# Performance work log

Hardware: AMD Instinct MI355X
Metric: run time of the kernel (lower is better)

Reference implementation:

```python
import jax, jax.numpy as jnp
import numpy as np

G, K = 4, 3
P = K * K  # n_offset_points


def _conv(x, w, b, groups=1):
    # x: [B,C,H,W] NCHW, w: [O, I/groups, kh, kw] (torch OIHW), padding=1 -> SAME
    y = jax.lax.conv_general_dilated(x, w, (1, 1), 'SAME', feature_group_count=groups)
    return y + b[None, :, None, None]


def setup_inputs() -> dict:
    key = jax.random.key(0)
    ks = jax.random.split(key, 9)
    B, C, H, W = 4, 256, 64, 64
    Cg = C // G
    s = 0.05
    return {
        'x': jax.random.normal(ks[0], (B, H * W, C), jnp.float32),
        'off_w1': jax.random.normal(ks[1], (C, Cg, 3, 3), jnp.float32) * s,
        'off_b1': jax.random.normal(ks[2], (C,), jnp.float32) * s,
        'off_w2': jax.random.normal(ks[3], (G * 2 * P, C, 3, 3), jnp.float32) * s,
        'off_b2': jax.random.normal(ks[4], (G * 2 * P,), jnp.float32) * s,
        'mod_w1': jax.random.normal(ks[5], (C // 4, C, 3, 3), jnp.float32) * s,
        'mod_b1': jax.random.normal(ks[6], (C // 4,), jnp.float32) * s,
        'mod_w2': jax.random.normal(ks[7], (G * P, C // 4, 3, 3), jnp.float32) * s,
        'mod_b2': jax.random.normal(ks[8], (G * P,), jnp.float32) * s,
        'H': 64,
        'W': 64,
    }


def reference(x, off_w1, off_b1, off_w2, off_b2, mod_w1, mod_b1, mod_w2, mod_b2, H, W):
    B, N, C = x.shape
    Cg = C // G
    x2d = x.transpose(0, 2, 1).reshape(B, C, H, W)

    # offset branch (grouped 3x3 conv -> GELU -> 3x3 conv), offset_scale = 1.0
    h = jax.nn.gelu(_conv(x2d, off_w1, off_b1, groups=G), approximate=False)
    off = _conv(h, off_w2, off_b2).reshape(B, G, 2, P, H, W)
    # modulation branch
    m = jax.nn.gelu(_conv(x2d, mod_w1, mod_b1), approximate=False)
    mod = jax.nn.sigmoid(_conv(m, mod_w2, mod_b2)).reshape(B, G, P, H, W)

    # base kernel offsets: base[0]=x, base[1]=y, each [P]
    rv = jnp.arange(-(K - 1) // 2, (K - 1) // 2 + 1, dtype=x.dtype)
    by, bx = jnp.meshgrid(rv, rv, indexing='ij')
    bx, by = bx.reshape(P), by.reshape(P)

    yg, xg = jnp.meshgrid(jnp.arange(H, dtype=x.dtype), jnp.arange(W, dtype=x.dtype), indexing='ij')
    # sampling coords in pixel space; clamp to [-1,1] normalized (align_corners=True)
    # is exactly clamp to [0, W-1] / [0, H-1] in pixel space, and border padding
    # then never goes out of range.
    px = jnp.clip(xg + bx[:, None, None] + off[:, :, 0], 0.0, W - 1)  # [B,G,P,H,W]
    py = jnp.clip(yg + by[:, None, None] + off[:, :, 1], 0.0, H - 1)

    x0f, y0f = jnp.floor(px), jnp.floor(py)
    wx, wy = px - x0f, py - y0f
    x0 = x0f.astype(jnp.int32)
    y0 = y0f.astype(jnp.int32)
    x1 = jnp.minimum(x0 + 1, W - 1)
    y1 = jnp.minimum(y0 + 1, H - 1)

    flat = x2d.reshape(B, G, Cg, H * W)

    def gather(yi, xi):
        idx = (yi * W + xi).reshape(B, G, 1, P, H * W)
        return jnp.take_along_axis(flat[:, :, :, None, :], idx, axis=-1)  # [B,G,Cg,P,HW]

    wxr = wx.reshape(B, G, 1, P, H * W)
    wyr = wy.reshape(B, G, 1, P, H * W)
    v = (gather(y0, x0) * (1 - wxr) * (1 - wyr)
         + gather(y0, x1) * wxr * (1 - wyr)
         + gather(y1, x0) * (1 - wxr) * wyr
         + gather(y1, x1) * wxr * wyr)
    v = v * mod.reshape(B, G, 1, P, H * W)
    out = v.mean(axis=3)  # average over offset points -> [B,G,Cg,HW]
    return out.reshape(B, C, H * W).transpose(0, 2, 1)
```

## Files before the change

kernel.cpp:

```cpp
#include <hip/hip_runtime.h>
#include <math.h>


#define SLAB 4369
#define AGAP 1056
#define APXS 40
#define AROW (66*APXS)
#define AHALF (6*AROW)

typedef __attribute__((ext_vector_type(8))) short short8;
typedef __attribute__((ext_vector_type(4))) float floatx4;

__device__ __forceinline__ unsigned short f2bf(float f) {
    unsigned u = __float_as_uint(f);
    u = (u + 0x7FFFu + ((u >> 16) & 1u)) >> 16;
    return (unsigned short)u;
}
__device__ __forceinline__ float bf2f(unsigned short h) {
    return __uint_as_float(((unsigned)h) << 16);
}
__device__ __forceinline__ void split2(float v, unsigned short* hi, unsigned short* lo) {
    unsigned short h = f2bf(v);
    *hi = h;
    *lo = f2bf(v - bf2f(h));
}
__device__ __forceinline__ float gelu_exact(float v) {
    return 0.5f * v * (1.0f + erff(v * 0.70710678118654752f));
}

template<int NC, int NTAPS, int NT, int ACT, int OUTMODE>
__device__ __forceinline__ void conv_core_lds(
    unsigned short* lds,
    const unsigned short* __restrict__ ah, const unsigned short* __restrict__ al,
    int aC0,
    const unsigned short* __restrict__ wh, const unsigned short* __restrict__ wl,
    const float* __restrict__ bias,
    int b, int mblock, int tap0,
    unsigned short* __restrict__ oh, unsigned short* __restrict__ ol,
    int oC0,
    float* __restrict__ pf)
{
    const int OCPAD = NT * 16;
    unsigned short* Ahl = lds;
    unsigned short* All = lds + AHALF;
    unsigned short* Bhl = lds + 2 * AHALF;
    unsigned short* Bll = lds + 2 * AHALF + OCPAD * APXS;

    int tid = (int)threadIdx.x;
    int wave = tid >> 6;
    int lane = tid & 63;
    int quad = lane >> 4;
    int l16 = lane & 15;

    int pix0 = (mblock * 4 + wave) * 64;
    int y0 = mblock * 4;

    floatx4 acc[4][NT];
#pragma unroll
    for (int nt = 0; nt < NT; nt++) {
        float bv = (OUTMODE == 1) ? bias[nt * 16 + l16] : 0.f;
#pragma unroll
        for (int mt = 0; mt < 4; mt++) { floatx4 v = {bv, bv, bv, bv}; acc[mt][nt] = v; }
    }

#pragma unroll 1
    for (int ch = 0; ch < NC; ch++) {
        {
            size_t gbase = ((size_t)((aC0 + ch) * 4 + b) * SLAB + (size_t)y0 * 66) * 32;
#pragma unroll
            for (int k = 0; k < 7; k++) {
                int u = k * 256 + tid;
                if (u < 1584) {
                    int px = u >> 2, j = u & 3;
                    int row = px / 66, col = px - row * 66;
                    int dst = row * AROW + col * APXS + j * 8;
                    *(short8*)(Ahl + dst) = *(const short8*)(ah + gbase + (size_t)u * 8);
                    *(short8*)(All + dst) = *(const short8*)(al + gbase + (size_t)u * 8);
                }
            }
        }
#pragma unroll 1
        for (int tp = 0; tp < NTAPS; tp++) {
            int tap = tap0 + tp;
            int kh = tap / 3, kw = tap - kh * 3;
            {
                size_t wbase = (size_t)(ch * 9 + tap) * OCPAD * 32;
                const int BU = OCPAD * 4;
#pragma unroll
                for (int k = 0; k * 256 < BU; k++) {
                    int u = k * 256 + tid;
                    if (u < BU) {
                        int oc = u >> 2, j = u & 3;
                        int dst = oc * APXS + j * 8;
                        *(short8*)(Bhl + dst) = *(const short8*)(wh + wbase + (size_t)u * 8);
                        *(short8*)(Bll + dst) = *(const short8*)(wl + wbase + (size_t)u * 8);
                    }
                }
            }
            __syncthreads();

            short8 Afh[4], Afl[4], Bfh[NT], Bfl[NT];
            int arow = (wave + kh) * AROW;
#pragma unroll
            for (int mt = 0; mt < 4; mt++) {
                int aoff = arow + (kw + l16 + mt * 16) * APXS + quad * 8;
                Afh[mt] = *(const short8*)(Ahl + aoff);
                Afl[mt] = *(const short8*)(All + aoff);
            }
#pragma unroll
            for (int nt = 0; nt < NT; nt++) {
                int boff = (nt * 16 + l16) * APXS + quad * 8;
                Bfh[nt] = *(const short8*)(Bhl + boff);
                Bfl[nt] = *(const short8*)(Bll + boff);
            }
#pragma unroll
            for (int nt = 0; nt < NT; nt++) {
#pragma unroll
                for (int mt = 0; mt < 4; mt++) {
                    acc[mt][nt] = __builtin_amdgcn_mfma_f32_16x16x32_bf16(Afh[mt], Bfh[nt], acc[mt][nt], 0, 0, 0);
                    acc[mt][nt] = __builtin_amdgcn_mfma_f32_16x16x32_bf16(Afh[mt], Bfl[nt], acc[mt][nt], 0, 0, 0);
                    acc[mt][nt] = __builtin_amdgcn_mfma_f32_16x16x32_bf16(Afl[mt], Bfh[nt], acc[mt][nt], 0, 0, 0);
                }
            }
            __syncthreads();
        }
    }

#pragma unroll
    for (int nt = 0; nt < NT; nt++) {
        int oc = nt * 16 + l16;
#pragma unroll
        for (int mt = 0; mt < 4; mt++) {
#pragma unroll
            for (int r = 0; r < 4; r++) {
                float v = acc[mt][nt][r];
                int px = pix0 + mt * 16 + quad * 4 + r;
                if (OUTMODE == 2) {
                    atomicAdd(pf + ((size_t)b * 4096 + px) * OCPAD + oc, v);
                } else if (OUTMODE == 3) {
                    pf[((size_t)b * 4096 + px) * OCPAD + oc] = v;
                } else {
                    if (ACT == 1) v = gelu_exact(v);
                    else if (ACT == 2) v = 1.0f / (1.0f + expf(-v));
                    int yy = (px >> 6) + 1, xx = (px & 63) + 1;
                    int och = oC0 + (oc >> 5);
                    size_t o = ((size_t)(och * 4 + b) * SLAB + yy * 66 + xx) * 32 + (oc & 31);
                    unsigned short hv, lv; split2(v, &hv, &lv);
                    oh[o] = hv; ol[o] = lv;
                }
            }
        }
    }
}

__global__ __launch_bounds__(256, 1) void convA_kernel(
    const unsigned short* __restrict__ xph, const unsigned short* __restrict__ xpl,
    const unsigned short* __restrict__ w1h, const unsigned short* __restrict__ w1l,
    const float* __restrict__ off_b1,
    const unsigned short* __restrict__ w3h, const unsigned short* __restrict__ w3l,
    unsigned short* __restrict__ h1h, unsigned short* __restrict__ h1l,
    float* __restrict__ P3)
{
    __shared__ unsigned short lds[2 * AHALF + 2 * 64 * APXS];
    int bx = blockIdx.x;
    int xcd = bx & 7;
    int j = bx >> 3;
    int pair = xcd * 8 + j / 7;
    int role = j % 7;
    int mb = pair & 15;
    int b = pair >> 4;
    if (role < 4) {
        int g = role;
        conv_core_lds<2, 9, 4, 1, 1>(lds, xph, xpl, g * 2,
            w1h + (size_t)g * 2 * 9 * 64 * 32, w1l + (size_t)g * 2 * 9 * 64 * 32,
            off_b1 + g * 64,
            b, mb, 0, h1h, h1l, g * 2, nullptr);
    } else {
        int ks = role - 4;
        conv_core_lds<8, 3, 4, 0, 2>(lds, xph, xpl, 0, w3h, w3l, nullptr,
            b, mb, ks * 3, nullptr, nullptr, 0, P3);
    }
}

__global__ __launch_bounds__(256) void finalizeA_kernel(
    const float* __restrict__ P3, const float* __restrict__ mod_b1,
    unsigned short* __restrict__ m1h, unsigned short* __restrict__ m1l)
{
    int idx = blockIdx.x * 256 + threadIdx.x;
    int c = idx & 63;
    int p = idx >> 6;
    int b = p >> 12;
    int px = p & 4095;
    int rem = ((px >> 6) + 1) * 66 + (px & 63) + 1;
    float u = P3[(size_t)p * 64 + c] + mod_b1[c];
    u = gelu_exact(u);
    size_t o = ((size_t)((c >> 5) * 4 + b) * SLAB + rem) * 32 + (c & 31);
    unsigned short hu, lu; split2(u, &hu, &lu);
    m1h[o] = hu; m1l[o] = lu;
}

__global__ __launch_bounds__(256, 1) void convB_kernel(
    const unsigned short* __restrict__ h1h, const unsigned short* __restrict__ h1l,
    const unsigned short* __restrict__ w2h, const unsigned short* __restrict__ w2l,
    const unsigned short* __restrict__ m1h, const unsigned short* __restrict__ m1l,
    const unsigned short* __restrict__ w4h, const unsigned short* __restrict__ w4l,
    float* __restrict__ P2a, float* __restrict__ P4a)
{
    __shared__ unsigned short lds[2 * AHALF + 2 * 80 * APXS];
    int bx = blockIdx.x;
    if (bx < 192) {
        int xcd = bx & 7;
        int j = bx >> 3;
        int pair = xcd * 8 + j / 3;
        int ks = j % 3;
        int mb = pair & 15;
        int b = pair >> 4;
        conv_core_lds<8, 3, 5, 0, 2>(lds, h1h, h1l, 0, w2h, w2l, nullptr,
            b, mb, ks * 3, nullptr, nullptr, 0, P2a);
    } else {
        int t = bx - 192;
        int xcd = t & 7;
        int q = t >> 3;
        int pair = xcd * 8 + q;
        int mb = pair & 15;
        int b = pair >> 4;
        conv_core_lds<2, 9, 3, 0, 3>(lds, m1h, m1l, 0, w4h, w4l, nullptr,
            b, mb, 0, nullptr, nullptr, 0, P4a);
    }
}

#define ZBLK 2304
#define RBLK 1040
#define XBLK 17424
#define WBLK 1980
__global__ void prep_all_kernel(
    const float* __restrict__ x,
    const float* __restrict__ w1f, const float* __restrict__ w2f,
    const float* __restrict__ w3f, const float* __restrict__ w4f,
    unsigned short* __restrict__ xph, unsigned short* __restrict__ xpl,
    unsigned short* __restrict__ h1h, unsigned short* __restrict__ h1l,
    unsigned short* __restrict__ m1h, unsigned short* __restrict__ m1l,
    unsigned short* __restrict__ w1h, unsigned short* __restrict__ w1l,
    unsigned short* __restrict__ w2h, unsigned short* __restrict__ w2l,
    unsigned short* __restrict__ w3h, unsigned short* __restrict__ w3l,
    unsigned short* __restrict__ w4h, unsigned short* __restrict__ w4l,
    float* __restrict__ accf)
{
    int blk = blockIdx.x;
    int t = threadIdx.x;
    if (blk < ZBLK) {
        ((uint4*)accf)[(size_t)blk * 256 + t] = make_uint4(0u, 0u, 0u, 0u);
        return;
    }
    blk -= ZBLK;
    if (blk < RBLK) {
        int b = blk / 260;
        int r = blk - b * 260;
        int i, j;
        if (r < 66)       { i = 0;        j = r; }
        else if (r < 132) { i = 65;       j = r - 66; }
        else if (r < 196) { i = r - 131;  j = 0; }
        else              { i = r - 195;  j = 65; }
        size_t pp = (size_t)i * 66 + j;
        int ch = t >> 5, sub = t & 31;
        size_t o = ((size_t)(ch * 4 + b) * SLAB + pp) * 32 + sub;
        h1h[o] = 0; h1l[o] = 0;
        if (t < 64) { m1h[o] = 0; m1l[o] = 0; }
        return;
    }
    blk -= RBLK;
    if (blk < XBLK) {
        int b = blk / 4356;
        int rem = blk - b * 4356;
        int i = rem / 66, j = rem - i * 66;
        float v = 0.f;
        if (i >= 1 && i <= 64 && j >= 1 && j <= 64)
            v = x[((size_t)b * 4096 + (size_t)(i - 1) * 64 + (j - 1)) * 256 + t];
        size_t o = ((size_t)((t >> 5) * 4 + b) * SLAB + rem) * 32 + (t & 31);
        unsigned short h, l; split2(v, &h, &l);
        xph[o] = h; xpl[o] = l;
        return;
    }
    blk -= XBLK;
    {
        const int N1 = 147456, N2 = 184320, N3 = 147456, N4 = 27648;
        int idx = blk * 256 + t;
        const float* w; unsigned short *outh, *outl;
        int ocpad, oc_real, ic, base;
        if (idx < N1)                { w = w1f; outh = w1h; outl = w1l; ocpad = 64; oc_real = 64; ic = 64;  base = 0; }
        else if (idx < N1 + N2)      { w = w2f; outh = w2h; outl = w2l; ocpad = 80; oc_real = 72; ic = 256; base = N1; }
        else if (idx < N1 + N2 + N3) { w = w3f; outh = w3h; outl = w3l; ocpad = 64; oc_real = 64; ic = 256; base = N1 + N2; }
        else                         { w = w4f; outh = w4h; outl = w4l; ocpad = 48; oc_real = 36; ic = 64;  base = N1 + N2 + N3; }
        int lidx = idx - base;
        int ici = lidx & 31;
        int t1 = lidx >> 5;
        int ocp = t1 % ocpad;
        int t2 = t1 / ocpad;
        int tap = t2 % 9;
        int t3 = t2 / 9;
        int nch = ic >> 5;
        int ch = t3 % nch;
        int g = t3 / nch;
        float v = 0.f;
        if (ocp < oc_real) {
            int oc = g * oc_real + ocp;
            int icx = ch * 32 + ici;
            v = w[((size_t)oc * ic + icx) * 9 + tap];
        }
        unsigned short h, l; split2(v, &h, &l);
        outh[lidx] = h; outl[lidx] = l;
    }
}

__global__ __launch_bounds__(256) void deform_sample(
    const float* __restrict__ x,
    const float* __restrict__ P2a, const float* __restrict__ P4a,
    const float* __restrict__ b2, const float* __restrict__ b4,
    float* __restrict__ out)
{
    int bid = (int)((blockIdx.x & 7u) * 512u + (blockIdx.x >> 3));
    int wid = (int)(((unsigned)bid * 256u + threadIdx.x) >> 6);
    int lane = (int)(threadIdx.x & 63u);
    int sub = lane >> 4;
    int li = lane & 15;

    int b = wid >> 12;
    int rem = wid & 4095;
    int g = rem >> 10;
    int hw = ((rem & 1023) << 2) + sub;
    int hy = hw >> 6;
    int wx = hw & 63;

    float fx = 0.f, fy = 0.f, fm = 0.f;
    if (li < 9) {
        size_t p = (size_t)(b << 12) + hw;
        int c2 = g * 18 + li;
        fx = P2a[p * 80 + c2] + b2[c2];
        fy = P2a[p * 80 + 9 + c2] + b2[9 + c2];
        int c4 = g * 9 + li;
        float mv = P4a[p * 48 + c4] + b4[c4];
        fm = 1.0f / (1.0f + expf(-mv));
    }
    float px = fminf(fmaxf((float)wx + (float)(li % 3 - 1) + fx, 0.f), 63.f);
    float py = fminf(fmaxf((float)hy + (float)(li / 3 - 1) + fy, 0.f), 63.f);
    float x0f = floorf(px), y0f = floorf(py);
    float wxf = px - x0f, wyf = py - y0f;
    int x0 = (int)x0f, y0 = (int)y0f;
    int x1 = min(x0 + 1, 63), y1 = min(y0 + 1, 63);

    const float4* xb = (const float4*)(x + ((size_t)(b << 12)) * 256 + g * 64 + li * 4);
    float4 acc = make_float4(0.f, 0.f, 0.f, 0.f);
    int sb = sub << 4;
#pragma unroll
    for (int q = 0; q < 9; q++) {
        int src = sb + q;
        int   qx0 = __shfl(x0, src);
        int   qx1 = __shfl(x1, src);
        int   qy0 = __shfl(y0, src);
        int   qy1 = __shfl(y1, src);
        float qwx = __shfl(wxf, src);
        float qwy = __shfl(wyf, src);
        float qm  = __shfl(fm, src);
        float4 v00 = xb[(size_t)(qy0 * 64 + qx0) * 64];
        float4 v01 = xb[(size_t)(qy0 * 64 + qx1) * 64];
        float4 v10 = xb[(size_t)(qy1 * 64 + qx0) * 64];
        float4 v11 = xb[(size_t)(qy1 * 64 + qx1) * 64];
        float w00 = (1.f - qwx) * (1.f - qwy);
        float w01 = qwx * (1.f - qwy);
        float w10 = (1.f - qwx) * qwy;
        float w11 = qwx * qwy;
        acc.x += qm * (v00.x * w00 + v01.x * w01 + v10.x * w10 + v11.x * w11);
        acc.y += qm * (v00.y * w00 + v01.y * w01 + v10.y * w10 + v11.y * w11);
        acc.z += qm * (v00.z * w00 + v01.z * w01 + v10.z * w10 + v11.z * w11);
        acc.w += qm * (v00.w * w00 + v01.w * w01 + v10.w * w10 + v11.w * w11);
    }
    const float s = 1.f / 9.f;
    acc.x *= s; acc.y *= s; acc.z *= s; acc.w *= s;
    float4* ob = (float4*)(out + ((size_t)(b << 12) + hw) * 256 + g * 64 + li * 4);
    *ob = acc;
}

extern "C" void kernel_launch(void* const* d_in, const int* in_sizes, int n_in,
                              void* d_out, int out_size, void* d_ws, size_t ws_size,
                              hipStream_t stream)
{
    const float* x      = (const float*)d_in[0];
    const float* off_w1 = (const float*)d_in[1];
    const float* off_b1 = (const float*)d_in[2];
    const float* off_w2 = (const float*)d_in[3];
    const float* off_b2 = (const float*)d_in[4];
    const float* mod_w1 = (const float*)d_in[5];
    const float* mod_b1 = (const float*)d_in[6];
    const float* mod_w2 = (const float*)d_in[7];
    const float* mod_b2 = (const float*)d_in[8];

    const size_t XP = 8u * 4u * SLAB * 32u;
    const size_t MP = 2u * 4u * SLAB * 32u;
    const size_t W1 = 4u * 2u * 9u * 64u * 32u;
    const size_t W2 = 8u * 9u * 80u * 32u;
    const size_t W3 = 8u * 9u * 64u * 32u;
    const size_t W4 = 2u * 9u * 48u * 32u;

    unsigned short* ws = (unsigned short*)d_ws;
    size_t o = 0;
    unsigned short* xph = ws + o; o += XP + AGAP;
    unsigned short* xpl = ws + o; o += XP + AGAP;
    unsigned short* h1h = ws + o; o += XP + AGAP;
    unsigned short* h1l = ws + o; o += XP + AGAP;
    unsigned short* m1h = ws + o; o += MP + AGAP;
    unsigned short* m1l = ws + o; o += MP + AGAP;
    unsigned short* w1h = ws + o; o += W1 + AGAP;
    unsigned short* w1l = ws + o; o += W1 + AGAP;
    unsigned short* w2h = ws + o; o += W2 + AGAP;
    unsigned short* w2l = ws + o; o += W2 + AGAP;
    unsigned short* w3h = ws + o; o += W3 + AGAP;
    unsigned short* w3l = ws + o; o += W3 + AGAP;
    unsigned short* w4h = ws + o; o += W4 + AGAP;
    unsigned short* w4l = ws + o; o += W4 + AGAP;
    o += o & 1;
    float* fbase = (float*)(ws + o);
    float* P3  = fbase;
    float* P2a = P3 + (size_t)4 * 4096 * 64;
    float* P4a = P2a + (size_t)4 * 4096 * 80;
    const size_t ACC_FLOATS = (size_t)4 * 4096 * (64 + 80 + 48);
    size_t need_bytes = o * 2 + ACC_FLOATS * 4;
    if (ws_size < need_bytes) return;

    prep_all_kernel<<<ZBLK + RBLK + XBLK + WBLK, 256, 0, stream>>>(
        x, off_w1, off_w2, mod_w1, mod_w2,
        xph, xpl, h1h, h1l, m1h, m1l,
        w1h, w1l, w2h, w2l, w3h, w3l, w4h, w4l, P3);

    convA_kernel<<<dim3(448, 1, 1), 256, 0, stream>>>(xph, xpl, w1h, w1l, off_b1,
                                                      w3h, w3l, h1h, h1l, P3);
    finalizeA_kernel<<<4096, 256, 0, stream>>>(P3, mod_b1, m1h, m1l);
    convB_kernel<<<dim3(256, 1, 1), 256, 0, stream>>>(h1h, h1l, w2h, w2l,
                                                      m1h, m1l, w4h, w4l, P2a, P4a);
    deform_sample<<<4096, 256, 0, stream>>>(x, P2a, P4a, off_b2, mod_b2, (float*)d_out);
}
```

Before: 216.6 us.

## Prefetch conv tiles through registers, double-buffer weights, split channels across more blocks

The conv core now issues global loads for the next channel's input tile and the next tap's weights into registers before running the current MFMAs. It then writes them to LDS afterwards, with weights double-buffered when BDBUF is set. Split-K blocks load only the 4 input rows they need. Both conv kernels split the channel dimension in half (and the mod_w2 conv by tap row), which raises grid sizes from 448/256 to 640/576 blocks. More blocks atomically add into the same outputs, so the zero-init block count grows. The cost is more register pressure and more atomic traffic.

New measurement: 224.7 us. 3.7% more time.

```diff
diff --git a/kernel.cpp b/kernel.cpp
--- a/kernel.cpp
+++ b/kernel.cpp
@@ -6,7 +6,6 @@
 #define AGAP 1056
 #define APXS 40
 #define AROW (66*APXS)
-#define AHALF (6*AROW)
 
 typedef __attribute__((ext_vector_type(8))) short short8;
 typedef __attribute__((ext_vector_type(4))) float floatx4;
@@ -28,12 +27,13 @@
     return 0.5f * v * (1.0f + erff(v * 0.70710678118654752f));
 }
 
-template<int NC, int NTAPS, int NT, int ACT, int OUTMODE>
+template<int NC, int NTAPS, int NT, int NROWS, int BDBUF, int ACT, int OUTMODE>
 __device__ __forceinline__ void conv_core_lds(
     unsigned short* lds,
     const unsigned short* __restrict__ ah, const unsigned short* __restrict__ al,
     int aC0,
     const unsigned short* __restrict__ wh, const unsigned short* __restrict__ wl,
+    int wC0,
     const float* __restrict__ bias,
     int b, int mblock, int tap0,
     unsigned short* __restrict__ oh, unsigned short* __restrict__ ol,
@@ -41,10 +41,17 @@
     float* __restrict__ pf)
 {
     const int OCPAD = NT * 16;
+    const int AHALFN = NROWS * AROW;
+    const int AU = NROWS * 66 * 4;
+    const int KA = (AU + 255) / 256;
+    const int BU = OCPAD * 4;
+    const int KB = (BU + 255) / 256;
+    const int BHALF = OCPAD * APXS;
+    const int BBUF = 2 * BHALF;
+
     unsigned short* Ahl = lds;
-    unsigned short* All = lds + AHALF;
-    unsigned short* Bhl = lds + 2 * AHALF;
-    unsigned short* Bll = lds + 2 * AHALF + OCPAD * APXS;
+    unsigned short* All = lds + AHALFN;
+    unsigned short* Bb  = lds + 2 * AHALFN;
 
     int tid = (int)threadIdx.x;
     int wave = tid >> 6;
@@ -52,8 +59,9 @@
     int quad = lane >> 4;
     int l16 = lane & 15;
 
+    int y0 = mblock * 4;
+    int row0 = (NROWS == 4) ? (tap0 / 3) : 0;
     int pix0 = (mblock * 4 + wave) * 64;
-    int y0 = mblock * 4;
 
     floatx4 acc[4][NT];
 #pragma unroll
@@ -63,44 +71,85 @@
         for (int mt = 0; mt < 4; mt++) { floatx4 v = {bv, bv, bv, bv}; acc[mt][nt] = v; }
     }
 
+    short8 ARh[KA], ARl[KA], BRh[KB], BRl[KB];
+
+    auto issueA = [&](int ch) {
+        size_t gbase = ((size_t)((aC0 + ch) * 4 + b) * SLAB + (size_t)(y0 + row0) * 66) * 32;
+#pragma unroll
+        for (int k = 0; k < KA; k++) {
+            int u = k * 256 + tid;
+            if (u < AU) {
+                ARh[k] = *(const short8*)(ah + gbase + (size_t)u * 8);
+                ARl[k] = *(const short8*)(al + gbase + (size_t)u * 8);
+            }
+        }
+    };
+    auto writeA = [&]() {
+#pragma unroll
+        for (int k = 0; k < KA; k++) {
+            int u = k * 256 + tid;
+            if (u < AU) {
+                int px = u >> 2, j = u & 3;
+                int row = px / 66, col = px - row * 66;
+                int dst = row * AROW + col * APXS + j * 8;
+                *(short8*)(Ahl + dst) = ARh[k];
+                *(short8*)(All + dst) = ARl[k];
+            }
+        }
+    };
+    auto issueB = [&](int it) {
+        int ch_ = it / NTAPS, tap_ = tap0 + it % NTAPS;
+        size_t wbase = ((size_t)((wC0 + ch_) * 9 + tap_)) * OCPAD * 32;
+#pragma unroll
+        for (int k = 0; k < KB; k++) {
+            int u = k * 256 + tid;
+            if (u < BU) {
+                BRh[k] = *(const short8*)(wh + wbase + (size_t)u * 8);
+                BRl[k] = *(const short8*)(wl + wbase + (size_t)u * 8);
+            }
+        }
+    };
+    auto writeB = [&](int sel) {
+        unsigned short* bh = Bb + sel * BBUF;
+        unsigned short* bl = bh + BHALF;
+#pragma unroll
+        for (int k = 0; k < KB; k++) {
+            int u = k * 256 + tid;
+            if (u < BU) {
+                int oc = u >> 2, j = u & 3;
+                int dst = oc * APXS + j * 8;
+                *(short8*)(bh + dst) = BRh[k];
+                *(short8*)(bl + dst) = BRl[k];
+            }
+        }
+    };
+
+    issueA(0);
+    issueB(0);
+    __builtin_amdgcn_sched_barrier(0);
+    writeA();
+    writeB(0);
+    __syncthreads();
+
+    int bsel = 0;
 #pragma unroll 1
     for (int ch = 0; ch < NC; ch++) {
-        {
-            size_t gbase = ((size_t)((aC0 + ch) * 4 + b) * SLAB + (size_t)y0 * 66) * 32;
-#pragma unroll
-            for (int k = 0; k < 7; k++) {
-                int u = k * 256 + tid;
-                if (u < 1584) {
-                    int px = u >> 2, j = u & 3;
-                    int row = px / 66, col = px - row * 66;
-                    int dst = row * AROW + col * APXS + j * 8;
-                    *(short8*)(Ahl + dst) = *(const short8*)(ah + gbase + (size_t)u * 8);
-                    *(short8*)(All + dst) = *(const short8*)(al + gbase + (size_t)u * 8);
-                }
-            }
-        }
-#pragma unroll 1
+#pragma unroll
         for (int tp = 0; tp < NTAPS; tp++) {
+            int it = ch * NTAPS + tp;
+            const bool chEnd = (tp == NTAPS - 1);
+            const bool lastIt = (ch == NC - 1) && chEnd;
+            if (!lastIt) {
+                if (chEnd) issueA(ch + 1);
+                issueB(it + 1);
+                __builtin_amdgcn_sched_barrier(0);
+            }
             int tap = tap0 + tp;
-            int kh = tap / 3, kw = tap - kh * 3;
-            {
-                size_t wbase = (size_t)(ch * 9 + tap) * OCPAD * 32;
-                const int BU = OCPAD * 4;
-#pragma unroll
-                for (int k = 0; k * 256 < BU; k++) {
-                    int u = k * 256 + tid;
-                    if (u < BU) {
-                        int oc = u >> 2, j = u & 3;
-                        int dst = oc * APXS + j * 8;
-                        *(short8*)(Bhl + dst) = *(const short8*)(wh + wbase + (size_t)u * 8);
-                        *(short8*)(Bll + dst) = *(const short8*)(wl + wbase + (size_t)u * 8);
-                    }
-                }
-            }
-            __syncthreads();
-
+            int kw = tap % 3;
+            int arow = ((NROWS == 6) ? (wave + tap / 3) : wave) * AROW;
+            unsigned short* bh = Bb + bsel * BBUF;
+            unsigned short* bl = bh + BHALF;
             short8 Afh[4], Afl[4], Bfh[NT], Bfl[NT];
-            int arow = (wave + kh) * AROW;
 #pragma unroll
             for (int mt = 0; mt < 4; mt++) {
                 int aoff = arow + (kw + l16 + mt * 16) * APXS + quad * 8;
@@ -110,8 +159,8 @@
 #pragma unroll
             for (int nt = 0; nt < NT; nt++) {
                 int boff = (nt * 16 + l16) * APXS + quad * 8;
-                Bfh[nt] = *(const short8*)(Bhl + boff);
-                Bfl[nt] = *(const short8*)(Bll + boff);
+                Bfh[nt] = *(const short8*)(bh + boff);
+                Bfl[nt] = *(const short8*)(bl + boff);
             }
 #pragma unroll
             for (int nt = 0; nt < NT; nt++) {
@@ -122,7 +171,20 @@
                     acc[mt][nt] = __builtin_amdgcn_mfma_f32_16x16x32_bf16(Afl[mt], Bfh[nt], acc[mt][nt], 0, 0, 0);
                 }
             }
-            __syncthreads();
+            if (!lastIt) {
+                if (BDBUF && !chEnd) {
+                    writeB(bsel ^ 1);
+                    __syncthreads();
+                    bsel ^= 1;
+                } else {
+                    __syncthreads();
+                    int ns = BDBUF ? (bsel ^ 1) : 0;
+                    writeB(ns);
+                    if (chEnd) writeA();
+                    __syncthreads();
+                    bsel = ns;
+                }
+            }
         }
     }
 
@@ -161,23 +223,25 @@
     unsigned short* __restrict__ h1h, unsigned short* __restrict__ h1l,
     float* __restrict__ P3)
 {
-    __shared__ unsigned short lds[2 * AHALF + 2 * 64 * APXS];
+    __shared__ unsigned short lds[36800];
     int bx = blockIdx.x;
     int xcd = bx & 7;
     int j = bx >> 3;
-    int pair = xcd * 8 + j / 7;
-    int role = j % 7;
+    int pair = xcd * 8 + j / 10;
+    int role = j % 10;
     int mb = pair & 15;
     int b = pair >> 4;
     if (role < 4) {
         int g = role;
-        conv_core_lds<2, 9, 4, 1, 1>(lds, xph, xpl, g * 2,
-            w1h + (size_t)g * 2 * 9 * 64 * 32, w1l + (size_t)g * 2 * 9 * 64 * 32,
+        conv_core_lds<2, 9, 4, 6, 0, 1, 1>(lds, xph, xpl, g * 2,
+            w1h + (size_t)g * 2 * 9 * 64 * 32, w1l + (size_t)g * 2 * 9 * 64 * 32, 0,
             off_b1 + g * 64,
             b, mb, 0, h1h, h1l, g * 2, nullptr);
     } else {
-        int ks = role - 4;
-        conv_core_lds<8, 3, 4, 0, 2>(lds, xph, xpl, 0, w3h, w3l, nullptr,
+        int r = role - 4;
+        int ks = r % 3, half = r / 3;
+        conv_core_lds<4, 3, 4, 4, 1, 0, 2>(lds, xph, xpl, half * 4,
+            w3h, w3l, half * 4, nullptr,
             b, mb, ks * 3, nullptr, nullptr, 0, P3);
     }
 }
@@ -206,30 +270,28 @@
     const unsigned short* __restrict__ w4h, const unsigned short* __restrict__ w4l,
     float* __restrict__ P2a, float* __restrict__ P4a)
 {
-    __shared__ unsigned short lds[2 * AHALF + 2 * 80 * APXS];
+    __shared__ unsigned short lds[33920];
     int bx = blockIdx.x;
-    if (bx < 192) {
-        int xcd = bx & 7;
-        int j = bx >> 3;
-        int pair = xcd * 8 + j / 3;
-        int ks = j % 3;
-        int mb = pair & 15;
-        int b = pair >> 4;
-        conv_core_lds<8, 3, 5, 0, 2>(lds, h1h, h1l, 0, w2h, w2l, nullptr,
+    int xcd = bx & 7;
+    int j = bx >> 3;
+    int pair = xcd * 8 + j / 9;
+    int role = j % 9;
+    int mb = pair & 15;
+    int b = pair >> 4;
+    if (role < 6) {
+        int ks = role % 3, half = role / 3;
+        conv_core_lds<4, 3, 5, 4, 1, 0, 2>(lds, h1h, h1l, half * 4,
+            w2h, w2l, half * 4, nullptr,
             b, mb, ks * 3, nullptr, nullptr, 0, P2a);
     } else {
-        int t = bx - 192;
-        int xcd = t & 7;
-        int q = t >> 3;
-        int pair = xcd * 8 + q;
-        int mb = pair & 15;
-        int b = pair >> 4;
-        conv_core_lds<2, 9, 3, 0, 3>(lds, m1h, m1l, 0, w4h, w4l, nullptr,
-            b, mb, 0, nullptr, nullptr, 0, P4a);
-    }
-}
-
-#define ZBLK 2304
+        int ks = role - 6;
+        conv_core_lds<2, 3, 3, 4, 1, 0, 2>(lds, m1h, m1l, 0,
+            w4h, w4l, 0, nullptr,
+            b, mb, ks * 3, nullptr, nullptr, 0, P4a);
+    }
+}
+
+#define ZBLK 3072
 #define RBLK 1040
 #define XBLK 17424
 #define WBLK 1980
@@ -431,10 +493,10 @@
         xph, xpl, h1h, h1l, m1h, m1l,
         w1h, w1l, w2h, w2l, w3h, w3l, w4h, w4l, P3);
 
-    convA_kernel<<<dim3(448, 1, 1), 256, 0, stream>>>(xph, xpl, w1h, w1l, off_b1,
+    convA_kernel<<<dim3(640, 1, 1), 256, 0, stream>>>(xph, xpl, w1h, w1l, off_b1,
                                                       w3h, w3l, h1h, h1l, P3);
     finalizeA_kernel<<<4096, 256, 0, stream>>>(P3, mod_b1, m1h, m1l);
-    convB_kernel<<<dim3(256, 1, 1), 256, 0, stream>>>(h1h, h1l, w2h, w2l,
+    convB_kernel<<<dim3(576, 1, 1), 256, 0, stream>>>(h1h, h1l, w2h, w2l,
                                                       m1h, m1l, w4h, w4l, P2a, P4a);
     deform_sample<<<4096, 256, 0, stream>>>(x, P2a, P4a, off_b2, mod_b2, (float*)d_out);
 }
```

## Pipeline conv stages per kernel row with register prefetch and split convB tiles

Applied to the files above, without the earlier changes.

Restructures the implicit-GEMM conv core so each stage loads one kernel row (one input row window plus three taps of weights) into LDS. The next stage is prefetched into registers while the current one runs MFMAs, which replaces the old per-tap load/sync loop. It also raises MFMA wave priority with setprio. convB now uses 2-row tiles and a balanced role mapping over 512 blocks, giving more parallelism. The costs are higher register pressure and extra barriers per stage.

Result: faster. 192.0 us (-11.4%).

```diff
diff --git a/kernel.cpp b/kernel.cpp
--- a/kernel.cpp
+++ b/kernel.cpp
@@ -6,7 +6,6 @@
 #define AGAP 1056
 #define APXS 40
 #define AROW (66*APXS)
-#define AHALF (6*AROW)
 
 typedef __attribute__((ext_vector_type(8))) short short8;
 typedef __attribute__((ext_vector_type(4))) float floatx4;
@@ -28,12 +27,13 @@
     return 0.5f * v * (1.0f + erff(v * 0.70710678118654752f));
 }
 
-template<int NC, int NTAPS, int NT, int ACT, int OUTMODE>
+template<int NC, int TG, int MT, int NT, int ACT, int OUTMODE>
 __device__ __forceinline__ void conv_core_lds(
     unsigned short* lds,
     const unsigned short* __restrict__ ah, const unsigned short* __restrict__ al,
     int aC0,
     const unsigned short* __restrict__ wh, const unsigned short* __restrict__ wl,
+    int wC0,
     const float* __restrict__ bias,
     int b, int mblock, int tap0,
     unsigned short* __restrict__ oh, unsigned short* __restrict__ ol,
@@ -41,10 +41,18 @@
     float* __restrict__ pf)
 {
     const int OCPAD = NT * 16;
+    const int NSTG = NC * TG;
+    const int AHALF_ = MT * AROW;
+    const int AU = MT * 66 * 4;
+    const int KA = (AU + 255) / 256;
+    const int BHALF_ = 3 * OCPAD * APXS;
+    const int BU = 3 * OCPAD * 4;
+    const int KB = (BU + 255) / 256;
+
     unsigned short* Ahl = lds;
-    unsigned short* All = lds + AHALF;
-    unsigned short* Bhl = lds + 2 * AHALF;
-    unsigned short* Bll = lds + 2 * AHALF + OCPAD * APXS;
+    unsigned short* All = lds + AHALF_;
+    unsigned short* Bhl = lds + 2 * AHALF_;
+    unsigned short* Bll = Bhl + BHALF_;
 
     int tid = (int)threadIdx.x;
     int wave = tid >> 6;
@@ -52,76 +60,109 @@
     int quad = lane >> 4;
     int l16 = lane & 15;
 
-    int pix0 = (mblock * 4 + wave) * 64;
-    int y0 = mblock * 4;
-
-    floatx4 acc[4][NT];
+    int pix0 = (mblock * 4 + wave) * (MT * 16);
+    int y0 = mblock * MT;
+    int lr = (MT == 4) ? wave : (wave >> 1);
+    int xb_ = (MT == 4) ? 0 : ((wave & 1) * 32);
+
+    floatx4 acc[MT][NT];
 #pragma unroll
     for (int nt = 0; nt < NT; nt++) {
         float bv = (OUTMODE == 1) ? bias[nt * 16 + l16] : 0.f;
 #pragma unroll
-        for (int mt = 0; mt < 4; mt++) { floatx4 v = {bv, bv, bv, bv}; acc[mt][nt] = v; }
-    }
+        for (int mt = 0; mt < MT; mt++) { floatx4 v = {bv, bv, bv, bv}; acc[mt][nt] = v; }
+    }
+
+    short8 ARh[KA], ARl[KA], BRh[KB], BRl[KB];
+
+    auto issueAB = [&](int s) {
+        int ch = s / TG;
+        int kh = (TG == 3) ? (s % 3) : (tap0 / 3);
+        size_t ga = ((size_t)((aC0 + ch) * 4 + b) * SLAB + (size_t)(y0 + kh) * 66) * 32;
+#pragma unroll
+        for (int k = 0; k < KA; k++) {
+            int u = k * 256 + tid;
+            if (u < AU) {
+                ARh[k] = *(const short8*)(ah + ga + (size_t)u * 8);
+                ARl[k] = *(const short8*)(al + ga + (size_t)u * 8);
+            }
+        }
+        size_t gb = ((size_t)((wC0 + ch) * 9 + kh * 3)) * OCPAD * 32;
+#pragma unroll
+        for (int k = 0; k < KB; k++) {
+            int u = k * 256 + tid;
+            if (u < BU) {
+                BRh[k] = *(const short8*)(wh + gb + (size_t)u * 8);
+                BRl[k] = *(const short8*)(wl + gb + (size_t)u * 8);
+            }
+        }
+    };
+    auto writeAB = [&]() {
+#pragma unroll
+        for (int k = 0; k < KA; k++) {
+            int u = k * 256 + tid;
+            if (u < AU) {
+                int px = u >> 2, j = u & 3;
+                int row = px / 66, col = px - row * 66;
+                int dst = row * AROW + col * APXS + j * 8;
+                *(short8*)(Ahl + dst) = ARh[k];
+                *(short8*)(All + dst) = ARl[k];
+            }
+        }
+#pragma unroll
+        for (int k = 0; k < KB; k++) {
+            int u = k * 256 + tid;
+            if (u < BU) {
+                int tp = u / (OCPAD * 4);
+                int r = u - tp * (OCPAD * 4);
+                int oc = r >> 2, j = u & 3;
+                int dst = tp * (OCPAD * APXS) + oc * APXS + j * 8;
+                *(short8*)(Bhl + dst) = BRh[k];
+                *(short8*)(Bll + dst) = BRl[k];
+            }
+        }
+    };
+
+    issueAB(0);
+    writeAB();
+    __syncthreads();
 
 #pragma unroll 1
-    for (int ch = 0; ch < NC; ch++) {
-        {
-            size_t gbase = ((size_t)((aC0 + ch) * 4 + b) * SLAB + (size_t)y0 * 66) * 32;
-#pragma unroll
-            for (int k = 0; k < 7; k++) {
-                int u = k * 256 + tid;
-                if (u < 1584) {
-                    int px = u >> 2, j = u & 3;
-                    int row = px / 66, col = px - row * 66;
-                    int dst = row * AROW + col * APXS + j * 8;
-                    *(short8*)(Ahl + dst) = *(const short8*)(ah + gbase + (size_t)u * 8);
-                    *(short8*)(All + dst) = *(const short8*)(al + gbase + (size_t)u * 8);
-                }
-            }
-        }
-#pragma unroll 1
-        for (int tp = 0; tp < NTAPS; tp++) {
-            int tap = tap0 + tp;
-            int kh = tap / 3, kw = tap - kh * 3;
-            {
-                size_t wbase = (size_t)(ch * 9 + tap) * OCPAD * 32;
-                const int BU = OCPAD * 4;
-#pragma unroll
-                for (int k = 0; k * 256 < BU; k++) {
-                    int u = k * 256 + tid;
-                    if (u < BU) {
-                        int oc = u >> 2, j = u & 3;
-                        int dst = oc * APXS + j * 8;
-                        *(short8*)(Bhl + dst) = *(const short8*)(wh + wbase + (size_t)u * 8);
-                        *(short8*)(Bll + dst) = *(const short8*)(wl + wbase + (size_t)u * 8);
-                    }
-                }
-            }
-            __syncthreads();
-
-            short8 Afh[4], Afl[4], Bfh[NT], Bfl[NT];
-            int arow = (wave + kh) * AROW;
-#pragma unroll
-            for (int mt = 0; mt < 4; mt++) {
-                int aoff = arow + (kw + l16 + mt * 16) * APXS + quad * 8;
+    for (int s = 0; s < NSTG; s++) {
+        if (s + 1 < NSTG) {
+            issueAB(s + 1);
+            __builtin_amdgcn_sched_barrier(0);
+        }
+#pragma unroll
+        for (int kw = 0; kw < 3; kw++) {
+            short8 Afh[MT], Afl[MT], Bfh[NT], Bfl[NT];
+#pragma unroll
+            for (int mt = 0; mt < MT; mt++) {
+                int aoff = lr * AROW + (xb_ + kw + l16 + mt * 16) * APXS + quad * 8;
                 Afh[mt] = *(const short8*)(Ahl + aoff);
                 Afl[mt] = *(const short8*)(All + aoff);
             }
 #pragma unroll
             for (int nt = 0; nt < NT; nt++) {
-                int boff = (nt * 16 + l16) * APXS + quad * 8;
+                int boff = kw * (OCPAD * APXS) + (nt * 16 + l16) * APXS + quad * 8;
                 Bfh[nt] = *(const short8*)(Bhl + boff);
                 Bfl[nt] = *(const short8*)(Bll + boff);
             }
+            __builtin_amdgcn_s_setprio(1);
 #pragma unroll
             for (int nt = 0; nt < NT; nt++) {
 #pragma unroll
-                for (int mt = 0; mt < 4; mt++) {
+                for (int mt = 0; mt < MT; mt++) {
                     acc[mt][nt] = __builtin_amdgcn_mfma_f32_16x16x32_bf16(Afh[mt], Bfh[nt], acc[mt][nt], 0, 0, 0);
                     acc[mt][nt] = __builtin_amdgcn_mfma_f32_16x16x32_bf16(Afh[mt], Bfl[nt], acc[mt][nt], 0, 0, 0);
                     acc[mt][nt] = __builtin_amdgcn_mfma_f32_16x16x32_bf16(Afl[mt], Bfh[nt], acc[mt][nt], 0, 0, 0);
                 }
             }
+            __builtin_amdgcn_s_setprio(0);
+        }
+        if (s + 1 < NSTG) {
+            __syncthreads();
+            writeAB();
             __syncthreads();
         }
     }
@@ -130,7 +171,7 @@
     for (int nt = 0; nt < NT; nt++) {
         int oc = nt * 16 + l16;
 #pragma unroll
-        for (int mt = 0; mt < 4; mt++) {
+        for (int mt = 0; mt < MT; mt++) {
 #pragma unroll
             for (int r = 0; r < 4; r++) {
                 float v = acc[mt][nt][r];
@@ -161,7 +202,7 @@
     unsigned short* __restrict__ h1h, unsigned short* __restrict__ h1l,
     float* __restrict__ P3)
 {
-    __shared__ unsigned short lds[2 * AHALF + 2 * 64 * APXS];
+    __shared__ unsigned short lds[36480];
     int bx = blockIdx.x;
     int xcd = bx & 7;
     int j = bx >> 3;
@@ -171,13 +212,14 @@
     int b = pair >> 4;
     if (role < 4) {
         int g = role;
-        conv_core_lds<2, 9, 4, 1, 1>(lds, xph, xpl, g * 2,
-            w1h + (size_t)g * 2 * 9 * 64 * 32, w1l + (size_t)g * 2 * 9 * 64 * 32,
+        conv_core_lds<2, 3, 4, 4, 1, 1>(lds, xph, xpl, g * 2,
+            w1h + (size_t)g * 2 * 9 * 64 * 32, w1l + (size_t)g * 2 * 9 * 64 * 32, 0,
             off_b1 + g * 64,
             b, mb, 0, h1h, h1l, g * 2, nullptr);
     } else {
         int ks = role - 4;
-        conv_core_lds<8, 3, 4, 0, 2>(lds, xph, xpl, 0, w3h, w3l, nullptr,
+        conv_core_lds<8, 1, 4, 4, 0, 2>(lds, xph, xpl, 0,
+            w3h, w3l, 0, nullptr,
             b, mb, ks * 3, nullptr, nullptr, 0, P3);
     }
 }
@@ -206,25 +248,21 @@
     const unsigned short* __restrict__ w4h, const unsigned short* __restrict__ w4l,
     float* __restrict__ P2a, float* __restrict__ P4a)
 {
-    __shared__ unsigned short lds[2 * AHALF + 2 * 80 * APXS];
+    __shared__ unsigned short lds[29760];
     int bx = blockIdx.x;
-    if (bx < 192) {
-        int xcd = bx & 7;
-        int j = bx >> 3;
-        int pair = xcd * 8 + j / 3;
-        int ks = j % 3;
-        int mb = pair & 15;
-        int b = pair >> 4;
-        conv_core_lds<8, 3, 5, 0, 2>(lds, h1h, h1l, 0, w2h, w2l, nullptr,
-            b, mb, ks * 3, nullptr, nullptr, 0, P2a);
+    int xcd = bx & 7;
+    int j = bx >> 3;
+    int pair = xcd * 16 + j / 4;
+    int role = j % 4;
+    int mb = pair & 31;
+    int b = pair >> 5;
+    if (role < 3) {
+        conv_core_lds<8, 1, 2, 5, 0, 2>(lds, h1h, h1l, 0,
+            w2h, w2l, 0, nullptr,
+            b, mb, role * 3, nullptr, nullptr, 0, P2a);
     } else {
-        int t = bx - 192;
-        int xcd = t & 7;
-        int q = t >> 3;
-        int pair = xcd * 8 + q;
-        int mb = pair & 15;
-        int b = pair >> 4;
-        conv_core_lds<2, 9, 3, 0, 3>(lds, m1h, m1l, 0, w4h, w4l, nullptr,
+        conv_core_lds<2, 3, 2, 3, 0, 3>(lds, m1h, m1l, 0,
+            w4h, w4l, 0, nullptr,
             b, mb, 0, nullptr, nullptr, 0, P4a);
     }
 }
@@ -434,7 +472,7 @@
     convA_kernel<<<dim3(448, 1, 1), 256, 0, stream>>>(xph, xpl, w1h, w1l, off_b1,
                                                       w3h, w3l, h1h, h1l, P3);
     finalizeA_kernel<<<4096, 256, 0, stream>>>(P3, mod_b1, m1h, m1l);
-    convB_kernel<<<dim3(256, 1, 1), 256, 0, stream>>>(h1h, h1l, w2h, w2l,
+    convB_kernel<<<dim3(512, 1, 1), 256, 0, stream>>>(h1h, h1l, w2h, w2l,
                                                       m1h, m1l, w4h, w4l, P2a, P4a);
     deform_sample<<<4096, 256, 0, stream>>>(x, P2a, P4a, off_b2, mod_b2, (float*)d_out);
 }
```
